# Optimization experiments

Hardware: AMD Instinct MI355X
Metric: run time of the kernel (lower is better)

The kernel has to match this reference:

```python
import jax, jax.numpy as jnp
import numpy as np

N = 131072   # number of query points
M = 8        # number of sub-models (2x2x2 ensemble grid)
H = 128      # hidden width of each sub-model MLP
GRID = np.array([2, 2, 2])  # model_grid_shape (data-dim order)


def _cell_extents():
    """Per-model [min,max] extents in x-coordinate order (x is flipped vs data dims)."""
    i = np.arange(M)
    c0 = i % GRID[0]
    c1 = (i // GRID[0]) % GRID[1]
    c2 = i // (GRID[0] * GRID[1])
    # flipped x coord j indexes grid dim j -> x-coord order is (c2, c1, c0)
    c_x = np.stack([c2, c1, c0], axis=-1).astype(np.float32)
    g_x = GRID[::-1].astype(np.float32)
    mins = -1.0 + 2.0 * c_x / g_x
    maxs = -1.0 + 2.0 * (c_x + 1.0) / g_x
    return mins.astype(np.float32), maxs.astype(np.float32)


def setup_inputs() -> dict:
    key = jax.random.key(0)
    ks = jax.random.split(key, 6)
    s = 0.1
    x = jax.random.uniform(ks[0], (N, 3), jnp.float32, -1.0, 1.0)
    W0 = jax.random.normal(ks[1], (M, 3, H), jnp.float32) * s
    b0 = jnp.zeros((M, H), jnp.float32)
    W1 = jax.random.normal(ks[2], (M, H, H), jnp.float32) * s
    b1 = jnp.zeros((M, H), jnp.float32)
    W2 = jax.random.normal(ks[3], (M, H, H), jnp.float32) * s
    b2 = jnp.zeros((M, H), jnp.float32)
    W3 = jax.random.normal(ks[4], (M, H, 1), jnp.float32) * s
    b3 = jnp.zeros((M, 1), jnp.float32)
    mins_np, maxs_np = _cell_extents()
    return {"x": x, "W0": W0, "b0": b0, "W1": W1, "b1": b1,
            "W2": W2, "b2": b2, "W3": W3, "b3": b3,
            "mins": jnp.asarray(mins_np), "maxs": jnp.asarray(maxs_np)}


def reference(x, W0, b0, W1, b1, W2, b2, W3, b3, mins, maxs):
    g = jnp.asarray(GRID, dtype=x.dtype)
    # per-point sub-model index (matches torch: flip(-1), scale by grid, linearize)
    u = (x + 1.0) / (2.0 + 1e-6)                      # [N,3] in [0,1)
    cell = (u[:, ::-1] * g).astype(jnp.int32)         # [N,3]
    idx = cell[:, 0] + cell[:, 1] * GRID[0] + cell[:, 2] * (GRID[0] * GRID[1])

    def step(y, p):
        i, w0, b0i, w1, b1i, w2, b2i, w3, b3i, mn, mx = p
        # normalize points into this model's local [-1,1]^3 box
        xn = -1.0 + 2.0 * (x - mn) / (mx - mn)        # [N,3]
        h = jax.nn.relu(xn @ w0 + b0i)                # [N,H]
        h = jax.nn.relu(h @ w1 + b1i)
        h = jax.nn.relu(h @ w2 + b2i)
        yi = h @ w3 + b3i                             # [N,1]
        y = jnp.where((idx == i)[:, None], yi, y)
        return y, None

    y0 = jnp.zeros((x.shape[0], 1), x.dtype)
    y, _ = jax.lax.scan(step, y0,
                        (jnp.arange(M), W0, b0, W1, b1, W2, b2, W3, b3, mins, maxs))
    return y
```

## Files before the change

### kernel.cpp

```cpp
#include <hip/hip_runtime.h>
#include <hip/hip_bf16.h>


#define HDIM 128
#define LDSH 136
#define TILE 64
#define NMODEL 8
#define TILES_X 272
#define SEGCAP 20480

typedef __bf16 bf16x8 __attribute__((ext_vector_type(8)));
typedef __bf16 bf16x4 __attribute__((ext_vector_type(4)));
typedef float  f32x4  __attribute__((ext_vector_type(4)));

__device__ __forceinline__ int model_of(float x0, float x1, float x2) {
  const float den = 2.000001f;
  float u0 = (x0 + 1.0f) / den;
  float u1 = (x1 + 1.0f) / den;
  float u2 = (x2 + 1.0f) / den;
  int c0 = (int)(u2 * 2.0f);
  int c1 = (int)(u1 * 2.0f);
  int c2 = (int)(u0 * 2.0f);
  return c0 + (c1 << 1) + (c2 << 2);
}

__global__ __launch_bounds__(256)
void srn_prep_scatter(const float* __restrict__ W1, const float* __restrict__ W2,
                      const float* __restrict__ x,
                      const float* __restrict__ mins, const float* __restrict__ maxs,
                      __bf16* __restrict__ Wt1, __bf16* __restrict__ Wt2,
                      int* __restrict__ cursors, f32x4* __restrict__ xperm, int N)
{
  const int b = blockIdx.x;
  const int tid = threadIdx.x;

  if (b < 64) {
    __shared__ float lds[64][65];
    const int m   = b >> 3;
    const int r2  = b & 7;
    const int mat = r2 >> 2;
    const int ti  = (r2 >> 1) & 1;
    const int tj  = r2 & 1;
    const float* src = (mat ? W2 : W1) + m * HDIM * HDIM;
    __bf16*      dst = (mat ? Wt2 : Wt1) + m * HDIM * HDIM;
    #pragma unroll
    for (int it = 0; it < 16; ++it) {
      const int rr = (tid >> 6) + it * 4, cc = tid & 63;
      lds[rr][cc] = src[(ti * 64 + rr) * HDIM + tj * 64 + cc];
    }
    __syncthreads();
    #pragma unroll
    for (int it = 0; it < 16; ++it) {
      const int nn = (tid >> 6) + it * 4, kk = tid & 63;
      dst[(tj * 64 + nn) * HDIM + ti * 64 + kk] = (__bf16)lds[kk][nn];
    }
  } else {
    __shared__ int lc[NMODEL], lb[NMODEL];
    __shared__ float mnS[NMODEL * 3], ivS[NMODEL * 3];
    if (tid < NMODEL) lc[tid] = 0;
    if (tid < NMODEL * 3) { mnS[tid] = mins[tid]; ivS[tid] = 2.0f / (maxs[tid] - mins[tid]); }
    __syncthreads();
    const int base = (b - 64) * 1024;
    int ids[4], rs[4];
    float px[4][3];
    #pragma unroll
    for (int it = 0; it < 4; ++it) {
      const int i = base + it * 256 + tid;
      if (i < N) {
        float x0 = x[3*i], x1 = x[3*i+1], x2 = x[3*i+2];
        px[it][0] = x0; px[it][1] = x1; px[it][2] = x2;
        ids[it] = model_of(x0, x1, x2);
        rs[it] = atomicAdd(&lc[ids[it]], 1);
      } else ids[it] = -1;
    }
    __syncthreads();
    if (tid < NMODEL) lb[tid] = lc[tid] ? atomicAdd(&cursors[tid], lc[tid]) : 0;
    __syncthreads();
    #pragma unroll
    for (int it = 0; it < 4; ++it) {
      if (ids[it] >= 0) {
        const int id = ids[it];
        const int i = base + it * 256 + tid;
        const int slot = lb[id] + rs[it];
        if (slot < SEGCAP) {
          f32x4 v;
          v[0] = -1.0f + (px[it][0] - mnS[3*id  ]) * ivS[3*id  ];
          v[1] = -1.0f + (px[it][1] - mnS[3*id+1]) * ivS[3*id+1];
          v[2] = -1.0f + (px[it][2] - mnS[3*id+2]) * ivS[3*id+2];
          v[3] = __int_as_float(i);
          xperm[(size_t)id * SEGCAP + slot] = v;
        }
      }
    }
  }
}

__global__ __launch_bounds__(256, 4)
void srn_main(const float* __restrict__ W0, const float* __restrict__ b0,
              const float* __restrict__ b1, const float* __restrict__ b2,
              const float* __restrict__ W3, const float* __restrict__ b3,
              const __bf16* __restrict__ Wt1, const __bf16* __restrict__ Wt2,
              const int* __restrict__ cursors, const f32x4* __restrict__ xperm,
              float* __restrict__ out, int N)
{
  __shared__ __align__(16) __bf16 hA[TILE * LDSH];
  __shared__ __align__(16) __bf16 hB[TILE * LDSH];
  __shared__ f32x4 xs4[TILE];
  __shared__ float w0s[3 * HDIM];
  __shared__ float b0s[HDIM];
  __shared__ float part[4][TILE];

  const int m = blockIdx.y;
  const int tid = threadIdx.x;
  const int lane = tid & 63;
  const int wave = tid >> 6;
  const int l16  = lane & 15;
  const int quad = lane >> 4;
  const int n0   = wave * 32;

  if (tid < HDIM) {
    w0s[tid]          = W0[m * 3 * HDIM + tid];
    w0s[HDIM + tid]   = W0[m * 3 * HDIM + HDIM + tid];
    w0s[2*HDIM + tid] = W0[m * 3 * HDIM + 2 * HDIM + tid];
    b0s[tid] = b0[m * HDIM + tid];
  }
  f32x4 b1r[2], b2r[2], w3r[2];
  #pragma unroll
  for (int nt = 0; nt < 2; ++nt) {
    const int nb = m * HDIM + n0 + nt * 16 + quad * 4;
    b1r[nt] = *(const f32x4*)(b1 + nb);
    b2r[nt] = *(const f32x4*)(b2 + nb);
    w3r[nt] = *(const f32x4*)(W3 + nb);
  }
  const int cnt = cursors[m];
  const float b3v = b3[m];
  const __bf16* Wt1m = Wt1 + m * HDIM * HDIM;
  const __bf16* Wt2m = Wt2 + m * HDIM * HDIM;
  const f32x4* xp = xperm + (size_t)m * SEGCAP;
  __syncthreads();

  for (int tile = blockIdx.x; tile * TILE < cnt; tile += gridDim.x) {
    const int base = tile * TILE;
    const int npts = min(TILE, cnt - base);

    if (tid < TILE) {
      f32x4 v;
      if (tid < npts) v = xp[base + tid];
      else { v[0] = 0.0f; v[1] = 0.0f; v[2] = 0.0f; v[3] = __int_as_float(-1); }
      xs4[tid] = v;
    }
    __syncthreads();

    {
      const int p  = lane;
      const int j0 = wave * 32;
      const f32x4 xv = xs4[p];
      #pragma unroll
      for (int jj = 0; jj < 32; jj += 8) {
        bf16x8 pk;
        #pragma unroll
        for (int u8 = 0; u8 < 8; u8 += 4) {
          const int j = j0 + jj + u8;
          f32x4 wa = *(const f32x4*)&w0s[j];
          f32x4 wb = *(const f32x4*)&w0s[HDIM + j];
          f32x4 wc = *(const f32x4*)&w0s[2*HDIM + j];
          f32x4 bb = *(const f32x4*)&b0s[j];
          #pragma unroll
          for (int u = 0; u < 4; ++u) {
            float v = fmaf(xv[0], wa[u], fmaf(xv[1], wb[u], fmaf(xv[2], wc[u], bb[u])));
            pk[u8 + u] = (__bf16)fmaxf(v, 0.0f);
          }
        }
        *(bf16x8*)(hA + p * LDSH + j0 + jj) = pk;
      }
    }
    __syncthreads();

    {
      f32x4 acc[2][4] = {};
      #pragma unroll
      for (int kk = 0; kk < 4; ++kk) {
        const int kOff = kk * 32 + quad * 8;
        bf16x8 a0 = *(const bf16x8*)(Wt1m + (n0 + l16) * HDIM + kOff);
        bf16x8 a1 = *(const bf16x8*)(Wt1m + (n0 + 16 + l16) * HDIM + kOff);
        #pragma unroll
        for (int pt = 0; pt < 4; ++pt) {
          bf16x8 bv = *(const bf16x8*)(hA + (pt * 16 + l16) * LDSH + kOff);
          acc[0][pt] = __builtin_amdgcn_mfma_f32_16x16x32_bf16(a0, bv, acc[0][pt], 0, 0, 0);
          acc[1][pt] = __builtin_amdgcn_mfma_f32_16x16x32_bf16(a1, bv, acc[1][pt], 0, 0, 0);
        }
      }
      #pragma unroll
      for (int nt = 0; nt < 2; ++nt) {
        #pragma unroll
        for (int pt = 0; pt < 4; ++pt) {
          bf16x4 pk;
          #pragma unroll
          for (int i = 0; i < 4; ++i)
            pk[i] = (__bf16)fmaxf(acc[nt][pt][i] + b1r[nt][i], 0.0f);
          *(bf16x4*)(hB + (pt * 16 + l16) * LDSH + n0 + nt * 16 + quad * 4) = pk;
        }
      }
    }
    __syncthreads();

    {
      f32x4 acc[2][4] = {};
      #pragma unroll
      for (int kk = 0; kk < 4; ++kk) {
        const int kOff = kk * 32 + quad * 8;
        bf16x8 a0 = *(const bf16x8*)(Wt2m + (n0 + l16) * HDIM + kOff);
        bf16x8 a1 = *(const bf16x8*)(Wt2m + (n0 + 16 + l16) * HDIM + kOff);
        #pragma unroll
        for (int pt = 0; pt < 4; ++pt) {
          bf16x8 bv = *(const bf16x8*)(hB + (pt * 16 + l16) * LDSH + kOff);
          acc[0][pt] = __builtin_amdgcn_mfma_f32_16x16x32_bf16(a0, bv, acc[0][pt], 0, 0, 0);
          acc[1][pt] = __builtin_amdgcn_mfma_f32_16x16x32_bf16(a1, bv, acc[1][pt], 0, 0, 0);
        }
      }
      #pragma unroll
      for (int pt = 0; pt < 4; ++pt) {
        float s = 0.0f;
        #pragma unroll
        for (int nt = 0; nt < 2; ++nt)
          #pragma unroll
          for (int i = 0; i < 4; ++i)
            s = fmaf(fmaxf(acc[nt][pt][i] + b2r[nt][i], 0.0f), w3r[nt][i], s);
        s += __shfl_xor(s, 16);
        s += __shfl_xor(s, 32);
        if (quad == 0) part[wave][pt * 16 + l16] = s;
      }
    }
    __syncthreads();

    if (tid < TILE) {
      const float y = part[0][tid] + part[1][tid] + part[2][tid] + part[3][tid] + b3v;
      const int p = __float_as_int(xs4[tid][3]);
      if (p >= 0) out[p] = y;
    }
  }
}

extern "C" void kernel_launch(void* const* d_in, const int* in_sizes, int n_in,
                              void* d_out, int out_size, void* d_ws, size_t ws_size,
                              hipStream_t stream)
{
  const float* x    = (const float*)d_in[0];
  const float* W0   = (const float*)d_in[1];
  const float* b0   = (const float*)d_in[2];
  const float* W1   = (const float*)d_in[3];
  const float* b1   = (const float*)d_in[4];
  const float* W2   = (const float*)d_in[5];
  const float* b2   = (const float*)d_in[6];
  const float* W3   = (const float*)d_in[7];
  const float* b3   = (const float*)d_in[8];
  const float* mins = (const float*)d_in[9];
  const float* maxs = (const float*)d_in[10];
  float* out = (float*)d_out;
  const int N = in_sizes[0] / 3;

  char* ws = (char*)d_ws;
  int* cursors = (int*)ws;
  f32x4* xperm = (f32x4*)(ws + 256);
  __bf16* Wt1  = (__bf16*)(ws + 256 + (size_t)16 * SEGCAP * NMODEL);
  __bf16* Wt2  = Wt1 + NMODEL * HDIM * HDIM;

  hipMemsetAsync(cursors, 0, NMODEL * sizeof(int), stream);
  const int sb = (N + 1023) >> 10;
  srn_prep_scatter<<<dim3(64 + sb), dim3(256), 0, stream>>>(
      W1, W2, x, mins, maxs, Wt1, Wt2, cursors, xperm, N);
  srn_main<<<dim3(TILES_X, NMODEL), dim3(256), 0, stream>>>(
      W0, b0, b1, b2, W3, b3, Wt1, Wt2, cursors, xperm, out, N);
}
```

Baseline: 115.8 us.

## Use wave-ballot binning, pad cursors, shrink main grid with prefetch

```diff
diff --git a/kernel.cpp b/kernel.cpp
--- a/kernel.cpp
+++ b/kernel.cpp
@@ -6,8 +6,9 @@
 #define LDSH 136
 #define TILE 64
 #define NMODEL 8
-#define TILES_X 272
+#define GRIDX 64
 #define SEGCAP 20480
+#define CURSTRIDE 16
 
 typedef __bf16 bf16x8 __attribute__((ext_vector_type(8)));
 typedef __bf16 bf16x4 __attribute__((ext_vector_type(4)));
@@ -55,41 +56,70 @@
       dst[(tj * 64 + nn) * HDIM + ti * 64 + kk] = (__bf16)lds[kk][nn];
     }
   } else {
-    __shared__ int lc[NMODEL], lb[NMODEL];
     __shared__ float mnS[NMODEL * 3], ivS[NMODEL * 3];
-    if (tid < NMODEL) lc[tid] = 0;
+    __shared__ int wtot[4][NMODEL], gbase[NMODEL], wpre[4][NMODEL];
     if (tid < NMODEL * 3) { mnS[tid] = mins[tid]; ivS[tid] = 2.0f / (maxs[tid] - mins[tid]); }
     __syncthreads();
-    const int base = (b - 64) * 1024;
-    int ids[4], rs[4];
-    float px[4][3];
+
+    const int lane = tid & 63;
+    const int wave = tid >> 6;
+    const unsigned long long mlt = (1ull << lane) - 1ull;
+    const int base = (b - 64) * 4096;
+
+    float qx[16][3];
+    int ids[16], offs[16];
+    int wc[NMODEL] = {};
+
     #pragma unroll
-    for (int it = 0; it < 4; ++it) {
+    for (int it = 0; it < 16; ++it) {
       const int i = base + it * 256 + tid;
-      if (i < N) {
-        float x0 = x[3*i], x1 = x[3*i+1], x2 = x[3*i+2];
-        px[it][0] = x0; px[it][1] = x1; px[it][2] = x2;
-        ids[it] = model_of(x0, x1, x2);
-        rs[it] = atomicAdd(&lc[ids[it]], 1);
-      } else ids[it] = -1;
-    }
-    __syncthreads();
-    if (tid < NMODEL) lb[tid] = lc[tid] ? atomicAdd(&cursors[tid], lc[tid]) : 0;
-    __syncthreads();
+      const float x0 = x[3*i], x1 = x[3*i+1], x2 = x[3*i+2];
+      const int id = model_of(x0, x1, x2);
+      ids[it] = id;
+      qx[it][0] = -1.0f + (x0 - mnS[3*id  ]) * ivS[3*id  ];
+      qx[it][1] = -1.0f + (x1 - mnS[3*id+1]) * ivS[3*id+1];
+      qx[it][2] = -1.0f + (x2 - mnS[3*id+2]) * ivS[3*id+2];
+      const unsigned long long bb0 = __ballot(id & 1);
+      const unsigned long long bb1 = __ballot(id & 2);
+      const unsigned long long bb2 = __ballot(id & 4);
+      const unsigned long long mym =
+          ((id & 1) ? bb0 : ~bb0) & ((id & 2) ? bb1 : ~bb1) & ((id & 4) ? bb2 : ~bb2);
+      const int rank = __popcll(mym & mlt);
+      int off = 0;
+      #pragma unroll
+      for (int mm = 0; mm < NMODEL; ++mm) {
+        const unsigned long long msk =
+            ((mm & 1) ? bb0 : ~bb0) & ((mm & 2) ? bb1 : ~bb1) & ((mm & 4) ? bb2 : ~bb2);
+        const int c = __popcll(msk);
+        if (id == mm) off = wc[mm] + rank;
+        wc[mm] += c;
+      }
+      offs[it] = off;
+    }
+
+    if (lane == 0) {
+      #pragma unroll
+      for (int mm = 0; mm < NMODEL; ++mm) wtot[wave][mm] = wc[mm];
+    }
+    __syncthreads();
+    if (tid < NMODEL) {
+      const int s0 = wtot[0][tid], s1 = wtot[1][tid], s2 = wtot[2][tid], s3 = wtot[3][tid];
+      const int tot = s0 + s1 + s2 + s3;
+      gbase[tid] = tot ? atomicAdd(&cursors[tid * CURSTRIDE], tot) : 0;
+      wpre[0][tid] = 0; wpre[1][tid] = s0; wpre[2][tid] = s0 + s1; wpre[3][tid] = s0 + s1 + s2;
+    }
+    __syncthreads();
+
     #pragma unroll
-    for (int it = 0; it < 4; ++it) {
-      if (ids[it] >= 0) {
-        const int id = ids[it];
-        const int i = base + it * 256 + tid;
-        const int slot = lb[id] + rs[it];
-        if (slot < SEGCAP) {
-          f32x4 v;
-          v[0] = -1.0f + (px[it][0] - mnS[3*id  ]) * ivS[3*id  ];
-          v[1] = -1.0f + (px[it][1] - mnS[3*id+1]) * ivS[3*id+1];
-          v[2] = -1.0f + (px[it][2] - mnS[3*id+2]) * ivS[3*id+2];
-          v[3] = __int_as_float(i);
-          xperm[(size_t)id * SEGCAP + slot] = v;
-        }
+    for (int it = 0; it < 16; ++it) {
+      const int i = base + it * 256 + tid;
+      const int id = ids[it];
+      const int slot = gbase[id] + wpre[wave][id] + offs[it];
+      if (slot < SEGCAP) {
+        f32x4 v;
+        v[0] = qx[it][0]; v[1] = qx[it][1]; v[2] = qx[it][2];
+        v[3] = __int_as_float(i);
+        xperm[(size_t)id * SEGCAP + slot] = v;
       }
     }
   }
@@ -132,24 +162,30 @@
     b2r[nt] = *(const f32x4*)(b2 + nb);
     w3r[nt] = *(const f32x4*)(W3 + nb);
   }
-  const int cnt = cursors[m];
+  const int cnt = cursors[m * CURSTRIDE];
   const float b3v = b3[m];
   const __bf16* Wt1m = Wt1 + m * HDIM * HDIM;
   const __bf16* Wt2m = Wt2 + m * HDIM * HDIM;
   const f32x4* xp = xperm + (size_t)m * SEGCAP;
   __syncthreads();
 
-  for (int tile = blockIdx.x; tile * TILE < cnt; tile += gridDim.x) {
-    const int base = tile * TILE;
-    const int npts = min(TILE, cnt - base);
+  f32x4 v;
+  int tile = blockIdx.x;
+  if (tid < TILE) {
+    const int idx = tile * TILE + tid;
+    if (idx < cnt) v = xp[idx];
+    else { v[0] = 0.0f; v[1] = 0.0f; v[2] = 0.0f; v[3] = __int_as_float(-1); }
+  }
+
+  for (; tile * TILE < cnt; tile += GRIDX) {
+    if (tid < TILE) xs4[tid] = v;
+    __syncthreads();
 
     if (tid < TILE) {
-      f32x4 v;
-      if (tid < npts) v = xp[base + tid];
+      const int idx = (tile + GRIDX) * TILE + tid;
+      if (idx < cnt) v = xp[idx];
       else { v[0] = 0.0f; v[1] = 0.0f; v[2] = 0.0f; v[3] = __int_as_float(-1); }
-      xs4[tid] = v;
-    }
-    __syncthreads();
+    }
 
     {
       const int p  = lane;
@@ -167,8 +203,8 @@
           f32x4 bb = *(const f32x4*)&b0s[j];
           #pragma unroll
           for (int u = 0; u < 4; ++u) {
-            float v = fmaf(xv[0], wa[u], fmaf(xv[1], wb[u], fmaf(xv[2], wc[u], bb[u])));
-            pk[u8 + u] = (__bf16)fmaxf(v, 0.0f);
+            float vv = fmaf(xv[0], wa[u], fmaf(xv[1], wb[u], fmaf(xv[2], wc[u], bb[u])));
+            pk[u8 + u] = (__bf16)fmaxf(vv, 0.0f);
           }
         }
         *(bf16x8*)(hA + p * LDSH + j0 + jj) = pk;
@@ -261,14 +297,13 @@
 
   char* ws = (char*)d_ws;
   int* cursors = (int*)ws;
-  f32x4* xperm = (f32x4*)(ws + 256);
-  __bf16* Wt1  = (__bf16*)(ws + 256 + (size_t)16 * SEGCAP * NMODEL);
+  f32x4* xperm = (f32x4*)(ws + 512);
+  __bf16* Wt1  = (__bf16*)(ws + 512 + (size_t)16 * SEGCAP * NMODEL);
   __bf16* Wt2  = Wt1 + NMODEL * HDIM * HDIM;
 
-  hipMemsetAsync(cursors, 0, NMODEL * sizeof(int), stream);
-  const int sb = (N + 1023) >> 10;
-  srn_prep_scatter<<<dim3(64 + sb), dim3(256), 0, stream>>>(
+  hipMemsetAsync(cursors, 0, NMODEL * CURSTRIDE * sizeof(int), stream);
+  srn_prep_scatter<<<dim3(64 + 32), dim3(256), 0, stream>>>(
       W1, W2, x, mins, maxs, Wt1, Wt2, cursors, xperm, N);
-  srn_main<<<dim3(TILES_X, NMODEL), dim3(256), 0, stream>>>(
+  srn_main<<<dim3(GRIDX, NMODEL), dim3(256), 0, stream>>>(
       W0, b0, b1, b2, W3, b3, Wt1, Wt2, cursors, xperm, out, N);
 }
```

Result: no change. 117.3 us (+1.3%).

## Fuse scatter and MLP into one kernel with in-block compaction and register-resident weights

Applied to the files above, without the earlier changes.

```diff
diff --git a/kernel.cpp b/kernel.cpp
--- a/kernel.cpp
+++ b/kernel.cpp
@@ -6,8 +6,8 @@
 #define LDSH 136
 #define TILE 64
 #define NMODEL 8
-#define TILES_X 272
-#define SEGCAP 20480
+#define NCHUNK 64
+#define RING 512
 
 typedef __bf16 bf16x8 __attribute__((ext_vector_type(8)));
 typedef __bf16 bf16x4 __attribute__((ext_vector_type(4)));
@@ -24,99 +24,34 @@
   return c0 + (c1 << 1) + (c2 << 2);
 }
 
-__global__ __launch_bounds__(256)
-void srn_prep_scatter(const float* __restrict__ W1, const float* __restrict__ W2,
-                      const float* __restrict__ x,
-                      const float* __restrict__ mins, const float* __restrict__ maxs,
-                      __bf16* __restrict__ Wt1, __bf16* __restrict__ Wt2,
-                      int* __restrict__ cursors, f32x4* __restrict__ xperm, int N)
-{
-  const int b = blockIdx.x;
-  const int tid = threadIdx.x;
-
-  if (b < 64) {
-    __shared__ float lds[64][65];
-    const int m   = b >> 3;
-    const int r2  = b & 7;
-    const int mat = r2 >> 2;
-    const int ti  = (r2 >> 1) & 1;
-    const int tj  = r2 & 1;
-    const float* src = (mat ? W2 : W1) + m * HDIM * HDIM;
-    __bf16*      dst = (mat ? Wt2 : Wt1) + m * HDIM * HDIM;
-    #pragma unroll
-    for (int it = 0; it < 16; ++it) {
-      const int rr = (tid >> 6) + it * 4, cc = tid & 63;
-      lds[rr][cc] = src[(ti * 64 + rr) * HDIM + tj * 64 + cc];
-    }
-    __syncthreads();
-    #pragma unroll
-    for (int it = 0; it < 16; ++it) {
-      const int nn = (tid >> 6) + it * 4, kk = tid & 63;
-      dst[(tj * 64 + nn) * HDIM + ti * 64 + kk] = (__bf16)lds[kk][nn];
-    }
-  } else {
-    __shared__ int lc[NMODEL], lb[NMODEL];
-    __shared__ float mnS[NMODEL * 3], ivS[NMODEL * 3];
-    if (tid < NMODEL) lc[tid] = 0;
-    if (tid < NMODEL * 3) { mnS[tid] = mins[tid]; ivS[tid] = 2.0f / (maxs[tid] - mins[tid]); }
-    __syncthreads();
-    const int base = (b - 64) * 1024;
-    int ids[4], rs[4];
-    float px[4][3];
-    #pragma unroll
-    for (int it = 0; it < 4; ++it) {
-      const int i = base + it * 256 + tid;
-      if (i < N) {
-        float x0 = x[3*i], x1 = x[3*i+1], x2 = x[3*i+2];
-        px[it][0] = x0; px[it][1] = x1; px[it][2] = x2;
-        ids[it] = model_of(x0, x1, x2);
-        rs[it] = atomicAdd(&lc[ids[it]], 1);
-      } else ids[it] = -1;
-    }
-    __syncthreads();
-    if (tid < NMODEL) lb[tid] = lc[tid] ? atomicAdd(&cursors[tid], lc[tid]) : 0;
-    __syncthreads();
-    #pragma unroll
-    for (int it = 0; it < 4; ++it) {
-      if (ids[it] >= 0) {
-        const int id = ids[it];
-        const int i = base + it * 256 + tid;
-        const int slot = lb[id] + rs[it];
-        if (slot < SEGCAP) {
-          f32x4 v;
-          v[0] = -1.0f + (px[it][0] - mnS[3*id  ]) * ivS[3*id  ];
-          v[1] = -1.0f + (px[it][1] - mnS[3*id+1]) * ivS[3*id+1];
-          v[2] = -1.0f + (px[it][2] - mnS[3*id+2]) * ivS[3*id+2];
-          v[3] = __int_as_float(i);
-          xperm[(size_t)id * SEGCAP + slot] = v;
-        }
-      }
-    }
-  }
-}
-
-__global__ __launch_bounds__(256, 4)
-void srn_main(const float* __restrict__ W0, const float* __restrict__ b0,
-              const float* __restrict__ b1, const float* __restrict__ b2,
-              const float* __restrict__ W3, const float* __restrict__ b3,
-              const __bf16* __restrict__ Wt1, const __bf16* __restrict__ Wt2,
-              const int* __restrict__ cursors, const f32x4* __restrict__ xperm,
-              float* __restrict__ out, int N)
+__global__ __launch_bounds__(256, 2)
+void srn_one(const float* __restrict__ W0, const float* __restrict__ b0,
+             const float* __restrict__ W1, const float* __restrict__ b1,
+             const float* __restrict__ W2, const float* __restrict__ b2,
+             const float* __restrict__ W3, const float* __restrict__ b3,
+             const float* __restrict__ x,
+             const float* __restrict__ mins, const float* __restrict__ maxs,
+             float* __restrict__ out, int N)
 {
   __shared__ __align__(16) __bf16 hA[TILE * LDSH];
   __shared__ __align__(16) __bf16 hB[TILE * LDSH];
+  __shared__ __align__(16) float wstage[32 * HDIM];
+  __shared__ f32x4 q[RING];
   __shared__ f32x4 xs4[TILE];
   __shared__ float w0s[3 * HDIM];
   __shared__ float b0s[HDIM];
   __shared__ float part[4][TILE];
-
-  const int m = blockIdx.y;
+  __shared__ int wsum[4];
+
+  const int m   = blockIdx.y;
+  const int bx  = blockIdx.x;
   const int tid = threadIdx.x;
   const int lane = tid & 63;
   const int wave = tid >> 6;
   const int l16  = lane & 15;
   const int quad = lane >> 4;
   const int n0   = wave * 32;
+  const unsigned long long mlt = (1ull << lane) - 1ull;
 
   if (tid < HDIM) {
     w0s[tid]          = W0[m * 3 * HDIM + tid];
@@ -132,20 +67,41 @@
     b2r[nt] = *(const f32x4*)(b2 + nb);
     w3r[nt] = *(const f32x4*)(W3 + nb);
   }
-  const int cnt = cursors[m];
   const float b3v = b3[m];
-  const __bf16* Wt1m = Wt1 + m * HDIM * HDIM;
-  const __bf16* Wt2m = Wt2 + m * HDIM * HDIM;
-  const f32x4* xp = xperm + (size_t)m * SEGCAP;
+  const float mn0 = mins[3*m], mn1 = mins[3*m+1], mn2 = mins[3*m+2];
+  const float iv0 = 2.0f / (maxs[3*m]   - mn0);
+  const float iv1 = 2.0f / (maxs[3*m+1] - mn1);
+  const float iv2 = 2.0f / (maxs[3*m+2] - mn2);
+
+  bf16x8 wf[2][2][4];
+  #pragma unroll
+  for (int mat = 0; mat < 2; ++mat) {
+    const float* Wsrc = (mat ? W2 : W1) + m * HDIM * HDIM;
+    #pragma unroll
+    for (int c = 0; c < 4; ++c) {
+      __syncthreads();
+      #pragma unroll
+      for (int it = 0; it < 4; ++it) {
+        const int idx = (it * 256 + tid) * 4;
+        *(f32x4*)&wstage[idx] = *(const f32x4*)&Wsrc[c * 32 * HDIM + idx];
+      }
+      __syncthreads();
+      #pragma unroll
+      for (int rr = 0; rr < 2; ++rr) {
+        bf16x8 pk;
+        #pragma unroll
+        for (int u = 0; u < 8; ++u)
+          pk[u] = (__bf16)wstage[(quad * 8 + u) * HDIM + n0 + rr * 16 + l16];
+        wf[mat][rr][c] = pk;
+      }
+    }
+  }
   __syncthreads();
 
-  for (int tile = blockIdx.x; tile * TILE < cnt; tile += gridDim.x) {
-    const int base = tile * TILE;
-    const int npts = min(TILE, cnt - base);
-
+  auto run_tile = [&](int qstart, int npts) {
     if (tid < TILE) {
       f32x4 v;
-      if (tid < npts) v = xp[base + tid];
+      if (tid < npts) v = q[(qstart + tid) & (RING - 1)];
       else { v[0] = 0.0f; v[1] = 0.0f; v[2] = 0.0f; v[3] = __int_as_float(-1); }
       xs4[tid] = v;
     }
@@ -161,14 +117,14 @@
         #pragma unroll
         for (int u8 = 0; u8 < 8; u8 += 4) {
           const int j = j0 + jj + u8;
-          f32x4 wa = *(const f32x4*)&w0s[j];
-          f32x4 wb = *(const f32x4*)&w0s[HDIM + j];
-          f32x4 wc = *(const f32x4*)&w0s[2*HDIM + j];
-          f32x4 bb = *(const f32x4*)&b0s[j];
+          f32x4 wa  = *(const f32x4*)&w0s[j];
+          f32x4 wb  = *(const f32x4*)&w0s[HDIM + j];
+          f32x4 wcv = *(const f32x4*)&w0s[2*HDIM + j];
+          f32x4 bb  = *(const f32x4*)&b0s[j];
           #pragma unroll
           for (int u = 0; u < 4; ++u) {
-            float v = fmaf(xv[0], wa[u], fmaf(xv[1], wb[u], fmaf(xv[2], wc[u], bb[u])));
-            pk[u8 + u] = (__bf16)fmaxf(v, 0.0f);
+            float vv = fmaf(xv[0], wa[u], fmaf(xv[1], wb[u], fmaf(xv[2], wcv[u], bb[u])));
+            pk[u8 + u] = (__bf16)fmaxf(vv, 0.0f);
           }
         }
         *(bf16x8*)(hA + p * LDSH + j0 + jj) = pk;
@@ -181,13 +137,11 @@
       #pragma unroll
       for (int kk = 0; kk < 4; ++kk) {
         const int kOff = kk * 32 + quad * 8;
-        bf16x8 a0 = *(const bf16x8*)(Wt1m + (n0 + l16) * HDIM + kOff);
-        bf16x8 a1 = *(const bf16x8*)(Wt1m + (n0 + 16 + l16) * HDIM + kOff);
         #pragma unroll
         for (int pt = 0; pt < 4; ++pt) {
           bf16x8 bv = *(const bf16x8*)(hA + (pt * 16 + l16) * LDSH + kOff);
-          acc[0][pt] = __builtin_amdgcn_mfma_f32_16x16x32_bf16(a0, bv, acc[0][pt], 0, 0, 0);
-          acc[1][pt] = __builtin_amdgcn_mfma_f32_16x16x32_bf16(a1, bv, acc[1][pt], 0, 0, 0);
+          acc[0][pt] = __builtin_amdgcn_mfma_f32_16x16x32_bf16(wf[0][0][kk], bv, acc[0][pt], 0, 0, 0);
+          acc[1][pt] = __builtin_amdgcn_mfma_f32_16x16x32_bf16(wf[0][1][kk], bv, acc[1][pt], 0, 0, 0);
         }
       }
       #pragma unroll
@@ -209,13 +163,11 @@
       #pragma unroll
       for (int kk = 0; kk < 4; ++kk) {
         const int kOff = kk * 32 + quad * 8;
-        bf16x8 a0 = *(const bf16x8*)(Wt2m + (n0 + l16) * HDIM + kOff);
-        bf16x8 a1 = *(const bf16x8*)(Wt2m + (n0 + 16 + l16) * HDIM + kOff);
         #pragma unroll
         for (int pt = 0; pt < 4; ++pt) {
           bf16x8 bv = *(const bf16x8*)(hB + (pt * 16 + l16) * LDSH + kOff);
-          acc[0][pt] = __builtin_amdgcn_mfma_f32_16x16x32_bf16(a0, bv, acc[0][pt], 0, 0, 0);
-          acc[1][pt] = __builtin_amdgcn_mfma_f32_16x16x32_bf16(a1, bv, acc[1][pt], 0, 0, 0);
+          acc[0][pt] = __builtin_amdgcn_mfma_f32_16x16x32_bf16(wf[1][0][kk], bv, acc[0][pt], 0, 0, 0);
+          acc[1][pt] = __builtin_amdgcn_mfma_f32_16x16x32_bf16(wf[1][1][kk], bv, acc[1][pt], 0, 0, 0);
         }
       }
       #pragma unroll
@@ -238,7 +190,44 @@
       const int p = __float_as_int(xs4[tid][3]);
       if (p >= 0) out[p] = y;
     }
-  }
+  };
+
+  const int cpb     = (((N + NCHUNK - 1) / NCHUNK) + 255) & ~255;
+  const int nchunks = cpb >> 8;
+  const int chunk0  = bx * cpb;
+  int qhead = 0, qtail = 0;
+
+  for (int c = 0; c < nchunks; ++c) {
+    const int i = chunk0 + c * 256 + tid;
+    bool sel = false;
+    f32x4 v;
+    if (i < N) {
+      const float x0 = x[3*i], x1 = x[3*i+1], x2 = x[3*i+2];
+      sel = (model_of(x0, x1, x2) == m);
+      if (sel) {
+        v[0] = fmaf(x0 - mn0, iv0, -1.0f);
+        v[1] = fmaf(x1 - mn1, iv1, -1.0f);
+        v[2] = fmaf(x2 - mn2, iv2, -1.0f);
+        v[3] = __int_as_float(i);
+      }
+    }
+    const unsigned long long bal = __ballot(sel);
+    const int wrank = __popcll(bal & mlt);
+    if (lane == 0) wsum[wave] = __popcll(bal);
+    __syncthreads();
+    int wbase = 0, total = 0;
+    #pragma unroll
+    for (int w = 0; w < 4; ++w) {
+      const int cw = wsum[w];
+      if (w < wave) wbase += cw;
+      total += cw;
+    }
+    if (sel) q[(qtail + wbase + wrank) & (RING - 1)] = v;
+    __syncthreads();
+    qtail += total;
+    while (qtail - qhead >= TILE) { run_tile(qhead, TILE); qhead += TILE; }
+  }
+  if (qtail > qhead) run_tile(qhead, qtail - qhead);
 }
 
 extern "C" void kernel_launch(void* const* d_in, const int* in_sizes, int n_in,
@@ -259,16 +248,6 @@
   float* out = (float*)d_out;
   const int N = in_sizes[0] / 3;
 
-  char* ws = (char*)d_ws;
-  int* cursors = (int*)ws;
-  f32x4* xperm = (f32x4*)(ws + 256);
-  __bf16* Wt1  = (__bf16*)(ws + 256 + (size_t)16 * SEGCAP * NMODEL);
-  __bf16* Wt2  = Wt1 + NMODEL * HDIM * HDIM;
-
-  hipMemsetAsync(cursors, 0, NMODEL * sizeof(int), stream);
-  const int sb = (N + 1023) >> 10;
-  srn_prep_scatter<<<dim3(64 + sb), dim3(256), 0, stream>>>(
-      W1, W2, x, mins, maxs, Wt1, Wt2, cursors, xperm, N);
-  srn_main<<<dim3(TILES_X, NMODEL), dim3(256), 0, stream>>>(
-      W0, b0, b1, b2, W3, b3, Wt1, Wt2, cursors, xperm, out, N);
+  srn_one<<<dim3(NCHUNK, NMODEL), dim3(256), 0, stream>>>(
+      W0, b0, W1, b1, W2, b2, W3, b3, x, mins, maxs, out, N);
 }
```

Measured after the change: 99.78 us. 1.16x faster.
